# Optimization experiments

Measured on AMD Instinct MI355X. Metric: run time of the kernel, lower is better.

Reference implementation:

```python
import jax, jax.numpy as jnp
import numpy as np

B, N, C = 2, 2048, 512
H = 8
HD = C // H


def _xavier(key, shape):
    fan_in, fan_out = shape[-1], shape[-2] if len(shape) > 1 else shape[-1]
    limit = float(np.sqrt(6.0 / (fan_in + fan_out)))
    return jax.random.uniform(key, shape, jnp.float32, -limit, limit)


def setup_inputs() -> dict:
    key = jax.random.key(0)
    ks = jax.random.split(key, 8)
    return {
        "x": jax.random.normal(ks[0], (B, N, C), jnp.float32),
        "pos_embedding": jax.random.normal(ks[1], (B, N, C), jnp.float32),
        "Wqkv": _xavier(ks[2], (3 * C, C)),      # nn.Linear(dim, 3*dim, bias=False)
        "Wpos": _xavier(ks[3], (C, C)),          # pos_proj, bias=False
        "u_bias": _xavier(ks[4], (H, HD)),
        "v_bias": _xavier(ks[5], (H, HD)),
        "Wproj": _xavier(ks[6], (C, C)),
        "bproj": jnp.zeros((C,), jnp.float32),
    }


def _relative_shift(ps):
    # ps: [B, H, N, M]
    b, h, n, m = ps.shape
    ps = jnp.pad(ps, ((0, 0), (0, 0), (0, 0), (1, 0)))  # zero column in front
    ps = ps.reshape(b, h, m + 1, n)[:, :, 1:, :]
    return ps.reshape(b, h, n, m)


def reference(x, pos_embedding, Wqkv, Wpos, u_bias, v_bias, Wproj, bproj):
    b, n, c = x.shape
    scale = HD ** -0.5
    qkv = (x @ Wqkv.T).reshape(b, n, 3, H, HD)
    q = qkv[:, :, 0].transpose(0, 2, 1, 3)  # [B,H,N,HD]
    k = qkv[:, :, 1].transpose(0, 2, 1, 3)
    v = qkv[:, :, 2].transpose(0, 2, 1, 3)
    pos = (pos_embedding @ Wpos.T).reshape(b, -1, H, HD)  # [B,M,H,HD]

    # content score: (q + u_bias) @ k^T -> [B,H,N,N]
    content = jnp.einsum("bhnd,bhmd->bhnm", q + u_bias[None, :, None, :], k)
    # pos score: (q + v_bias) @ pos^T -> [B,H,N,M]
    pos_score = jnp.einsum("bhnd,bmhd->bhnm", q + v_bias[None, :, None, :], pos)
    pos_score = _relative_shift(pos_score)

    attn = jax.nn.softmax((pos_score + content) * scale, axis=-1)
    out = jnp.einsum("bhnm,bhmd->bhnd", attn, v)
    out = out.transpose(0, 2, 1, 3).reshape(b, n, c)
    return out @ Wproj.T + bproj
```

## Files before the change

### kernel.cpp

```cpp
#include <hip/hip_runtime.h>

typedef __attribute__((ext_vector_type(8))) short bf16x8;
typedef __attribute__((ext_vector_type(4))) short bf16x4;
typedef __attribute__((ext_vector_type(4))) float f32x4;

__device__ __forceinline__ float bf2f(unsigned short u) {
  union { unsigned int i; float f; } c; c.i = ((unsigned int)u) << 16; return c.f;
}
__device__ __forceinline__ unsigned short f2bf(float x) {
  union { float f; unsigned int i; } c; c.f = x;
  return (unsigned short)((c.i + 0x7fffu + ((c.i >> 16) & 1u)) >> 16);
}
__device__ __forceinline__ unsigned int pk2(float a, float b) {
  return (unsigned int)f2bf(a) | ((unsigned int)f2bf(b) << 16);
}

__device__ __forceinline__ uint4 ld8f(const float* p) {
  const float4 a = *(const float4*)p;
  const float4 b = *(const float4*)(p + 4);
  uint4 r;
  r.x = (unsigned)f2bf(a.x) | ((unsigned)f2bf(a.y) << 16);
  r.y = (unsigned)f2bf(a.z) | ((unsigned)f2bf(a.w) << 16);
  r.z = (unsigned)f2bf(b.x) | ((unsigned)f2bf(b.y) << 16);
  r.w = (unsigned)f2bf(b.z) | ((unsigned)f2bf(b.w) << 16);
  return r;
}

__device__ __forceinline__ void gload16(const unsigned short* g, short* l) {
  __builtin_amdgcn_global_load_lds((const __attribute__((address_space(1))) void*)g,
                                   (__attribute__((address_space(3))) void*)l, 16, 0, 0);
}

__global__ __launch_bounds__(256) void k_cvt(const float* __restrict__ x,
    const float* __restrict__ pe, const float* __restrict__ wq,
    const float* __restrict__ wp, const float* __restrict__ wj,
    unsigned short* __restrict__ dst) {
  const long long i8 = ((long long)blockIdx.x * 256 + threadIdx.x) * 8;
  const float* src; long long off;
  if (i8 < 2097152)      { src = x;  off = i8; }
  else if (i8 < 4194304) { src = pe; off = i8 - 2097152; }
  else if (i8 < 4980736) { src = wq; off = i8 - 4194304; }
  else if (i8 < 5242880) { src = wp; off = i8 - 4980736; }
  else                   { src = wj; off = i8 - 5242880; }
  *(uint4*)&dst[i8] = ld8f(src + off);
}

__device__ __forceinline__ void gemm128_mainloop(const unsigned short* __restrict__ Arow,
                                                 const unsigned short* __restrict__ Wrow,
                                                 short* Asl, short* Wsl, f32x4 acc[4][4]) {
  const int tid = threadIdx.x, w = tid >> 6, lane = tid & 63, lm = lane & 15, lq = lane >> 4;
  const int wm = w >> 1, wn = w & 1;
  const int lrow = lane >> 3;
  const int gcol = (((lane & 7) ^ lrow) * 8);
#pragma unroll
  for (int mt = 0; mt < 4; ++mt)
#pragma unroll
    for (int nt = 0; nt < 4; ++nt) acc[mt][nt] = (f32x4){0.f, 0.f, 0.f, 0.f};
#pragma unroll 1
  for (int kc = 0; kc < 512; kc += 64) {
    __syncthreads();
#pragma unroll
    for (int ld = 0; ld < 4; ++ld) {
      const int rbase = w * 32 + ld * 8;
      gload16(&Arow[(size_t)(rbase + lrow) * 512 + kc + gcol], &Asl[rbase * 64]);
      gload16(&Wrow[(size_t)(rbase + lrow) * 512 + kc + gcol], &Wsl[rbase * 64]);
    }
    __syncthreads();
#pragma unroll
    for (int kk = 0; kk < 2; ++kk) {
      const int pcs = ((kk * 4 + lq) ^ (lm & 7)) * 8;
      bf16x8 af[4], bfr[4];
#pragma unroll
      for (int mt = 0; mt < 4; ++mt)
        af[mt] = *(const bf16x8*)&Asl[(wm * 64 + mt * 16 + lm) * 64 + pcs];
#pragma unroll
      for (int nt = 0; nt < 4; ++nt)
        bfr[nt] = *(const bf16x8*)&Wsl[(wn * 64 + nt * 16 + lm) * 64 + pcs];
#pragma unroll
      for (int mt = 0; mt < 4; ++mt)
#pragma unroll
        for (int nt = 0; nt < 4; ++nt)
          acc[mt][nt] = __builtin_amdgcn_mfma_f32_16x16x32_bf16(af[mt], bfr[nt], acc[mt][nt], 0, 0, 0);
    }
  }
}

__global__ __launch_bounds__(256) void k_gemm_qkvpos(const unsigned short* __restrict__ xb,
    const unsigned short* __restrict__ peb, const unsigned short* __restrict__ wqb,
    const unsigned short* __restrict__ wpb, const float* __restrict__ ub,
    const float* __restrict__ vb, unsigned short* __restrict__ qu,
    unsigned short* __restrict__ qv, unsigned short* __restrict__ kg,
    unsigned short* __restrict__ vg, unsigned short* __restrict__ pos) {
  __shared__ short Asl[128 * 64], Wsl[128 * 64];
  f32x4 acc[4][4];
  const int m0 = blockIdx.y * 128, cc0 = blockIdx.x * 128;
  const unsigned short* Arow = (cc0 < 1536 ? xb : peb) + (size_t)m0 * 512;
  const unsigned short* Wrow = (cc0 < 1536) ? (wqb + (size_t)cc0 * 512)
                                            : (wpb + (size_t)(cc0 - 1536) * 512);
  gemm128_mainloop(Arow, Wrow, Asl, Wsl, acc);
  const int tid = threadIdx.x, w = tid >> 6, lane = tid & 63, lm = lane & 15, lq = lane >> 4;
  const int wm = w >> 1, wn = w & 1;
#pragma unroll
  for (int nt = 0; nt < 4; ++nt) {
    const int cc = cc0 + wn * 64 + nt * 16 + lm;
    const int sec = cc >> 9, rem = cc & 511, h = rem >> 6, d = rem & 63;
#pragma unroll
    for (int mt = 0; mt < 4; ++mt) {
#pragma unroll
      for (int r = 0; r < 4; ++r) {
        const int m = m0 + wm * 64 + mt * 16 + lq * 4 + r;
        const int b = m >> 11, n = m & 2047;
        const size_t idx = ((size_t)(b * 8 + h) * 2048 + n) * 64 + d;
        const float val = acc[mt][nt][r];
        if (sec == 0) {
          qu[idx] = f2bf(val + ub[rem]);
          qv[idx] = f2bf(val + vb[rem]);
        } else if (sec == 1) {
          kg[idx] = f2bf(val);
        } else if (sec == 2) {
          vg[idx] = f2bf(val);
        } else {
          pos[idx] = f2bf(val);
        }
      }
    }
  }
}

__global__ __launch_bounds__(256) void k_transpose_v(const unsigned short* __restrict__ vg,
                                                     unsigned short* __restrict__ vt) {
  __shared__ short T[64][72];
  const int tid = threadIdx.x, bhid = blockIdx.y, n0 = blockIdx.x * 64;
#pragma unroll
  for (int s = 0; s < 2; ++s) {
    int u = tid + s * 256, row = u >> 3, c8 = (u & 7) * 8;
    *(uint4*)&T[row][c8] = *(const uint4*)&vg[((size_t)bhid * 2048 + n0 + row) * 64 + c8];
  }
  __syncthreads();
#pragma unroll
  for (int s = 0; s < 2; ++s) {
    int u = tid + s * 256, d = u >> 3, n8 = (u & 7) * 8;
    alignas(16) unsigned short tmp[8];
#pragma unroll
    for (int jj = 0; jj < 8; ++jj) tmp[jj] = (unsigned short)T[n8 + jj][d];
    *(uint4*)&vt[((size_t)bhid * 64 + d) * 2048 + n0 + n8] = *(const uint4*)tmp;
  }
}

__global__ __launch_bounds__(256, 2) void k_flash(const unsigned short* __restrict__ qu,
    const unsigned short* __restrict__ qv, const unsigned short* __restrict__ kg,
    const unsigned short* __restrict__ vt, const unsigned short* __restrict__ posg,
    unsigned short* __restrict__ og) {
  __shared__ short SB[23892];
  short* Ks = SB;
  short* Vs = SB + 4608;
  short* Pn = SB + 9216;
  short* T  = SB + 18432;
  float* Ored = (float*)SB;
  const int tid = threadIdx.x, w = tid >> 6, lane = tid & 63, lm = lane & 15, lq = lane >> 4;
  const int bh = blockIdx.y, i0 = blockIdx.x * 64;
  const size_t bhs = (size_t)bh;
  const unsigned short* qub = qu + bhs * (2048 * 64);
  const unsigned short* qvb = qv + bhs * (2048 * 64);
  const unsigned short* pob = posg + bhs * (2048 * 64);
  bf16x8 au[4][2];
#pragma unroll
  for (int qt = 0; qt < 4; ++qt) {
    au[qt][0] = *(const bf16x8*)&qub[(size_t)(i0 + qt * 16 + lm) * 64 + lq * 8];
    au[qt][1] = *(const bf16x8*)&qub[(size_t)(i0 + qt * 16 + lm) * 64 + 32 + lq * 8];
  }
  const bf16x8 av0 = *(const bf16x8*)&qvb[(size_t)(i0 + w * 16 + lm) * 64 + lq * 8];
  const bf16x8 av1 = *(const bf16x8*)&qvb[(size_t)(i0 + w * 16 + lm) * 64 + 32 + lq * 8];
  const int rowe = min(i0 + 49 + lm, 2047);
  const bf16x8 ae0 = *(const bf16x8*)&qvb[(size_t)rowe * 64 + lq * 8];
  const bf16x8 ae1 = *(const bf16x8*)&qvb[(size_t)rowe * 64 + 32 + lq * 8];
  float lsum[4] = {0.f, 0.f, 0.f, 0.f};
  f32x4 oacc[4][4];
#pragma unroll
  for (int ii = 0; ii < 4; ++ii)
#pragma unroll
    for (int jj = 0; jj < 4; ++jj) oacc[ii][jj] = (f32x4){0.f, 0.f, 0.f, 0.f};
  const int krow = tid >> 3, kc8 = (tid & 7) * 8;
  const int pb0 = 1983 - i0;
  uint4 kr0 = *(const uint4*)&kg[(bhs * 2048 + krow) * 64 + kc8];
  uint4 kr1 = *(const uint4*)&kg[(bhs * 2048 + krow + 32) * 64 + kc8];
  uint4 vr0 = *(const uint4*)&vt[(bhs * 64 + krow) * 2048 + kc8];
  uint4 vr1 = *(const uint4*)&vt[(bhs * 64 + krow + 32) * 2048 + kc8];
  uint4 pr[4];
#pragma unroll
  for (int s = 0; s < 4; ++s) {
    int u = tid + s * 256, prow = u >> 3, c8 = (u & 7) * 8;
    int grow = (pb0 + prow + 4096) & 2047;
    pr[s] = *(const uint4*)&pob[(size_t)grow * 64 + c8];
  }
#pragma unroll 1
  for (int jt = 0; jt < 32; ++jt) {
    const int j0 = jt * 64;
    const int pb = pb0 + j0;
    __syncthreads();
    *(uint4*)&Ks[krow * 72 + kc8] = kr0;
    *(uint4*)&Ks[(krow + 32) * 72 + kc8] = kr1;
    *(uint4*)&Vs[krow * 72 + kc8] = vr0;
    *(uint4*)&Vs[(krow + 32) * 72 + kc8] = vr1;
    if (jt == 0) {
#pragma unroll
      for (int s = 0; s < 4; ++s) {
        int u = tid + s * 256, prow = u >> 3, c8 = (u & 7) * 8;
        int slot = (pb + prow) & 127;
        *(uint4*)&Pn[slot * 72 + c8] = pr[s];
      }
    } else {
#pragma unroll
      for (int s = 0; s < 2; ++s) {
        int u = tid + s * 256, prow = u >> 3, c8 = (u & 7) * 8;
        int slot = (pb + 64 + prow) & 127;
        *(uint4*)&Pn[slot * 72 + c8] = pr[s];
      }
    }
    __syncthreads();
    if (jt < 31) {
      const int jn = j0 + 64;
      kr0 = *(const uint4*)&kg[(bhs * 2048 + jn + krow) * 64 + kc8];
      kr1 = *(const uint4*)&kg[(bhs * 2048 + jn + krow + 32) * 64 + kc8];
      vr0 = *(const uint4*)&vt[(bhs * 64 + krow) * 2048 + jn + kc8];
      vr1 = *(const uint4*)&vt[(bhs * 64 + krow + 32) * 2048 + jn + kc8];
#pragma unroll
      for (int s = 0; s < 2; ++s) {
        int u = tid + s * 256, prow = u >> 3, c8 = (u & 7) * 8;
        int grow = (pb + 128 + prow + 4096) & 2047;
        pr[s] = *(const uint4*)&pob[(size_t)grow * 64 + c8];
      }
    }
    const bf16x8 k0 = *(const bf16x8*)&Ks[(w * 16 + lm) * 72 + lq * 8];
    const bf16x8 k1 = *(const bf16x8*)&Ks[(w * 16 + lm) * 72 + 32 + lq * 8];
    f32x4 cacc[4];
#pragma unroll
    for (int qt = 0; qt < 4; ++qt) {
      cacc[qt] = __builtin_amdgcn_mfma_f32_16x16x32_bf16(k0, au[qt][0], (f32x4){0.f,0.f,0.f,0.f}, 0, 0, 0);
      cacc[qt] = __builtin_amdgcn_mfma_f32_16x16x32_bf16(k1, au[qt][1], cacc[qt], 0, 0, 0);
    }
    const int sbase = 49 - w * 16;
#pragma unroll
    for (int ct = 0; ct < 5; ++ct) {
      const int slot = (pb + sbase + ct * 16 + lm) & 127;
      const bf16x8 b0 = *(const bf16x8*)&Pn[slot * 72 + lq * 8];
      const bf16x8 b1 = *(const bf16x8*)&Pn[slot * 72 + 32 + lq * 8];
      f32x4 t0 = __builtin_amdgcn_mfma_f32_16x16x32_bf16(b0, av0, (f32x4){0.f,0.f,0.f,0.f}, 0, 0, 0);
      t0 = __builtin_amdgcn_mfma_f32_16x16x32_bf16(b1, av1, t0, 0, 0, 0);
      uint2 pk; pk.x = pk2(t0[0], t0[1]); pk.y = pk2(t0[2], t0[3]);
      *(uint2*)&T[(w * 16 + lm) * 84 + ct * 16 + lq * 4] = pk;
    }
    {
      const int slot = (pb + w * 16 + lm) & 127;
      const bf16x8 b0 = *(const bf16x8*)&Pn[slot * 72 + lq * 8];
      const bf16x8 b1 = *(const bf16x8*)&Pn[slot * 72 + 32 + lq * 8];
      f32x4 e0 = __builtin_amdgcn_mfma_f32_16x16x32_bf16(b0, ae0, (f32x4){0.f,0.f,0.f,0.f}, 0, 0, 0);
      e0 = __builtin_amdgcn_mfma_f32_16x16x32_bf16(b1, ae1, e0, 0, 0, 0);
      if (lm == 15) {
        uint2 pk; pk.x = pk2(e0[0], e0[1]); pk.y = pk2(e0[2], e0[3]);
        *(uint2*)&T[64 * 84 + w * 16 + lq * 4] = pk;
      }
    }
    __syncthreads();
    const int diag = i0 - j0;
    const int jl0 = w * 16 + lq * 4;
    bf16x4 pf[4];
    if (diag >= 64 || diag <= -128) {
      const int du = (diag <= -128) ? 1 : 0;
      const int rm = lm + du;
#pragma unroll
      for (int qt = 0; qt < 4; ++qt) {
        const int rowa = qt * 16 + rm;
        const int base = (rowa == 64) ? (64 * 84 + jl0)
                                      : (rowa * 84 + 15 + jl0 - (rm & 15));
#pragma unroll
        for (int r = 0; r < 4; ++r) {
          const float pv = bf2f((unsigned short)T[base + r]);
          const float p = exp2f((cacc[qt][r] + pv) * 0.18033688f);
          lsum[qt] += p;
          pf[qt][r] = (short)f2bf(p);
        }
      }
    } else {
#pragma unroll
      for (int qt = 0; qt < 4; ++qt) {
#pragma unroll
        for (int r = 0; r < 4; ++r) {
          const int jl = jl0 + r;
          const int d = (j0 - i0) + jl - (qt * 16 + lm);
          float pv;
          if (d == 1) {
            pv = 0.f;
          } else {
            const int rm2 = lm + ((d > 1) ? 1 : 0);
            const int rowa = qt * 16 + rm2;
            const int base = (rowa == 64) ? (64 * 84 + jl)
                                          : (rowa * 84 + 15 + jl - (rm2 & 15));
            pv = bf2f((unsigned short)T[base]);
          }
          const float p = exp2f((cacc[qt][r] + pv) * 0.18033688f);
          lsum[qt] += p;
          pf[qt][r] = (short)f2bf(p);
        }
      }
    }
#pragma unroll
    for (int dt = 0; dt < 4; ++dt) {
      const bf16x4 vf = *(const bf16x4*)&Vs[(dt * 16 + lm) * 72 + w * 16 + lq * 4];
#pragma unroll
      for (int qt = 0; qt < 4; ++qt)
        oacc[qt][dt] = __builtin_amdgcn_mfma_f32_16x16x16bf16_1k(pf[qt], vf, oacc[qt][dt], 0, 0, 0);
    }
  }
#pragma unroll
  for (int qt = 0; qt < 4; ++qt) {
    lsum[qt] += __shfl_xor(lsum[qt], 16, 64);
    lsum[qt] += __shfl_xor(lsum[qt], 32, 64);
  }
  __syncthreads();
  if (w == 0) {
#pragma unroll
    for (int qt = 0; qt < 4; ++qt) {
#pragma unroll
      for (int dt = 0; dt < 4; ++dt)
        *(f32x4*)&Ored[(dt * 16 + lm) * 68 + qt * 16 + lq * 4] = oacc[qt][dt];
      if (lq == 0) Ored[64 * 68 + qt * 16 + lm] = lsum[qt];
    }
  }
  __syncthreads();
#pragma unroll 1
  for (int ww = 1; ww < 4; ++ww) {
    if (w == ww) {
#pragma unroll
      for (int qt = 0; qt < 4; ++qt) {
#pragma unroll
        for (int dt = 0; dt < 4; ++dt) {
          f32x4 o = *(const f32x4*)&Ored[(dt * 16 + lm) * 68 + qt * 16 + lq * 4];
          o += oacc[qt][dt];
          *(f32x4*)&Ored[(dt * 16 + lm) * 68 + qt * 16 + lq * 4] = o;
        }
        if (lq == 0) Ored[64 * 68 + qt * 16 + lm] += lsum[qt];
      }
    }
    __syncthreads();
  }
  const int b = bh >> 3, h = bh & 7;
  const f32x4 lv = *(const f32x4*)&Ored[64 * 68 + w * 16 + lq * 4];
  f32x4 inv;
#pragma unroll
  for (int r = 0; r < 4; ++r) inv[r] = 1.f / lv[r];
#pragma unroll
  for (int dt = 0; dt < 4; ++dt) {
    const f32x4 o = *(const f32x4*)&Ored[(dt * 16 + lm) * 68 + w * 16 + lq * 4];
#pragma unroll
    for (int r = 0; r < 4; ++r)
      og[((size_t)b * 2048 + i0 + w * 16 + lq * 4 + r) * 512 + h * 64 + dt * 16 + lm] =
          f2bf(o[r] * inv[r]);
  }
}

__global__ __launch_bounds__(256) void k_gemm_proj(const unsigned short* __restrict__ og,
    const unsigned short* __restrict__ wjb, const float* __restrict__ bproj,
    float* __restrict__ out) {
  __shared__ short Asl[128 * 64], Wsl[128 * 64];
  f32x4 acc[4][4];
  const int m0 = blockIdx.y * 128, cc0 = blockIdx.x * 128;
  gemm128_mainloop(og + (size_t)m0 * 512, wjb + (size_t)cc0 * 512, Asl, Wsl, acc);
  const int tid = threadIdx.x, w = tid >> 6, lane = tid & 63, lm = lane & 15, lq = lane >> 4;
  const int wm = w >> 1, wn = w & 1;
#pragma unroll
  for (int nt = 0; nt < 4; ++nt) {
    const int cc = cc0 + wn * 64 + nt * 16 + lm;
    const float bias = bproj[cc];
#pragma unroll
    for (int mt = 0; mt < 4; ++mt) {
#pragma unroll
      for (int r = 0; r < 4; ++r) {
        const int m = m0 + wm * 64 + mt * 16 + lq * 4 + r;
        out[(size_t)m * 512 + cc] = acc[mt][nt][r] + bias;
      }
    }
  }
}

extern "C" void kernel_launch(void* const* d_in, const int* in_sizes, int n_in,
                              void* d_out, int out_size, void* d_ws, size_t ws_size,
                              hipStream_t stream) {
  const float* x     = (const float*)d_in[0];
  const float* pe    = (const float*)d_in[1];
  const float* wqkv  = (const float*)d_in[2];
  const float* wpos  = (const float*)d_in[3];
  const float* ub    = (const float*)d_in[4];
  const float* vb    = (const float*)d_in[5];
  const float* wproj = (const float*)d_in[6];
  const float* bproj = (const float*)d_in[7];
  float* out = (float*)d_out;
  unsigned short* ws = (unsigned short*)d_ws;

  const size_t SZ = (size_t)2 * 8 * 2048 * 64;
  unsigned short* qu   = ws;
  unsigned short* qv   = qu + SZ;
  unsigned short* kg   = qv + SZ;
  unsigned short* vg   = kg + SZ;
  unsigned short* vt   = vg + SZ;
  unsigned short* pos  = vt + SZ;
  unsigned short* og   = pos + SZ;
  unsigned short* cvtb = og + SZ;
  unsigned short* xb   = cvtb;
  unsigned short* peb  = cvtb + 2097152;
  unsigned short* wqb  = cvtb + 4194304;
  unsigned short* wpb  = cvtb + 4980736;
  unsigned short* wjb  = cvtb + 5242880;

  dim3 blk(256);
  hipLaunchKernelGGL(k_cvt,         dim3(2688),   blk, 0, stream, x, pe, wqkv, wpos, wproj, cvtb);
  hipLaunchKernelGGL(k_gemm_qkvpos, dim3(16, 32), blk, 0, stream,
                     xb, peb, wqb, wpb, ub, vb, qu, qv, kg, vg, pos);
  hipLaunchKernelGGL(k_transpose_v, dim3(32, 16), blk, 0, stream, vg, vt);
  hipLaunchKernelGGL(k_flash,       dim3(32, 16), blk, 0, stream, qu, qv, kg, vt, pos, og);
  hipLaunchKernelGGL(k_gemm_proj,   dim3(4, 32),  blk, 0, stream, og, wjb, bproj, out);
}
```

Measured before the change: 227.0 us.

## Halve flash query tile, drop pos LDS ring, remap blocks for locality

Shrinks the flash attention query tile from 64 to 32 rows, doubling the grid to 1024 blocks and raising the occupancy hint to 4 blocks per CU with a smaller shared buffer. The staged positional-embedding ring buffer in LDS is removed; waves read pos rows straight from global memory and split the relative-position MFMA work between wave pairs. Block indices are remapped so neighbouring blocks share a head pair, aiming at better cache reuse. The costs are that K/V tiles are loaded twice as often per query row and pos reads go through global/L2 instead of LDS.

```diff
diff --git a/kernel.cpp b/kernel.cpp
--- a/kernel.cpp
+++ b/kernel.cpp
@@ -147,37 +147,40 @@
   }
 }
 
-__global__ __launch_bounds__(256, 2) void k_flash(const unsigned short* __restrict__ qu,
+__global__ __launch_bounds__(256, 4) void k_flash(const unsigned short* __restrict__ qu,
     const unsigned short* __restrict__ qv, const unsigned short* __restrict__ kg,
     const unsigned short* __restrict__ vt, const unsigned short* __restrict__ posg,
     unsigned short* __restrict__ og) {
-  __shared__ short SB[23892];
+  __shared__ short SB[11988];
   short* Ks = SB;
   short* Vs = SB + 4608;
-  short* Pn = SB + 9216;
-  short* T  = SB + 18432;
+  short* T  = SB + 9216;
   float* Ored = (float*)SB;
   const int tid = threadIdx.x, w = tid >> 6, lane = tid & 63, lm = lane & 15, lq = lane >> 4;
-  const int bh = blockIdx.y, i0 = blockIdx.x * 64;
+  const int hw = blockIdx.x + 64 * blockIdx.y;
+  const int idx = hw >> 3;
+  const int bh = (hw & 7) * 2 + (idx & 1);
+  const int i0 = (idx >> 1) * 32;
   const size_t bhs = (size_t)bh;
   const unsigned short* qub = qu + bhs * (2048 * 64);
   const unsigned short* qvb = qv + bhs * (2048 * 64);
   const unsigned short* pob = posg + bhs * (2048 * 64);
-  bf16x8 au[4][2];
-#pragma unroll
-  for (int qt = 0; qt < 4; ++qt) {
+  bf16x8 au[2][2];
+#pragma unroll
+  for (int qt = 0; qt < 2; ++qt) {
     au[qt][0] = *(const bf16x8*)&qub[(size_t)(i0 + qt * 16 + lm) * 64 + lq * 8];
     au[qt][1] = *(const bf16x8*)&qub[(size_t)(i0 + qt * 16 + lm) * 64 + 32 + lq * 8];
   }
-  const bf16x8 av0 = *(const bf16x8*)&qvb[(size_t)(i0 + w * 16 + lm) * 64 + lq * 8];
-  const bf16x8 av1 = *(const bf16x8*)&qvb[(size_t)(i0 + w * 16 + lm) * 64 + 32 + lq * 8];
-  const int rowe = min(i0 + 49 + lm, 2047);
+  const int sw = w >> 1, ph = w & 1;
+  const bf16x8 av0 = *(const bf16x8*)&qvb[(size_t)(i0 + sw * 16 + lm) * 64 + lq * 8];
+  const bf16x8 av1 = *(const bf16x8*)&qvb[(size_t)(i0 + sw * 16 + lm) * 64 + 32 + lq * 8];
+  const int rowe = min(i0 + 17 + lm, 2047);
   const bf16x8 ae0 = *(const bf16x8*)&qvb[(size_t)rowe * 64 + lq * 8];
   const bf16x8 ae1 = *(const bf16x8*)&qvb[(size_t)rowe * 64 + 32 + lq * 8];
-  float lsum[4] = {0.f, 0.f, 0.f, 0.f};
-  f32x4 oacc[4][4];
-#pragma unroll
-  for (int ii = 0; ii < 4; ++ii)
+  float lsum[2] = {0.f, 0.f};
+  f32x4 oacc[2][4];
+#pragma unroll
+  for (int ii = 0; ii < 2; ++ii)
 #pragma unroll
     for (int jj = 0; jj < 4; ++jj) oacc[ii][jj] = (f32x4){0.f, 0.f, 0.f, 0.f};
   const int krow = tid >> 3, kc8 = (tid & 7) * 8;
@@ -186,13 +189,6 @@
   uint4 kr1 = *(const uint4*)&kg[(bhs * 2048 + krow + 32) * 64 + kc8];
   uint4 vr0 = *(const uint4*)&vt[(bhs * 64 + krow) * 2048 + kc8];
   uint4 vr1 = *(const uint4*)&vt[(bhs * 64 + krow + 32) * 2048 + kc8];
-  uint4 pr[4];
-#pragma unroll
-  for (int s = 0; s < 4; ++s) {
-    int u = tid + s * 256, prow = u >> 3, c8 = (u & 7) * 8;
-    int grow = (pb0 + prow + 4096) & 2047;
-    pr[s] = *(const uint4*)&pob[(size_t)grow * 64 + c8];
-  }
 #pragma unroll 1
   for (int jt = 0; jt < 32; ++jt) {
     const int j0 = jt * 64;
@@ -202,21 +198,6 @@
     *(uint4*)&Ks[(krow + 32) * 72 + kc8] = kr1;
     *(uint4*)&Vs[krow * 72 + kc8] = vr0;
     *(uint4*)&Vs[(krow + 32) * 72 + kc8] = vr1;
-    if (jt == 0) {
-#pragma unroll
-      for (int s = 0; s < 4; ++s) {
-        int u = tid + s * 256, prow = u >> 3, c8 = (u & 7) * 8;
-        int slot = (pb + prow) & 127;
-        *(uint4*)&Pn[slot * 72 + c8] = pr[s];
-      }
-    } else {
-#pragma unroll
-      for (int s = 0; s < 2; ++s) {
-        int u = tid + s * 256, prow = u >> 3, c8 = (u & 7) * 8;
-        int slot = (pb + 64 + prow) & 127;
-        *(uint4*)&Pn[slot * 72 + c8] = pr[s];
-      }
-    }
     __syncthreads();
     if (jt < 31) {
       const int jn = j0 + 64;
@@ -224,54 +205,63 @@
       kr1 = *(const uint4*)&kg[(bhs * 2048 + jn + krow + 32) * 64 + kc8];
       vr0 = *(const uint4*)&vt[(bhs * 64 + krow) * 2048 + jn + kc8];
       vr1 = *(const uint4*)&vt[(bhs * 64 + krow + 32) * 2048 + jn + kc8];
-#pragma unroll
-      for (int s = 0; s < 2; ++s) {
-        int u = tid + s * 256, prow = u >> 3, c8 = (u & 7) * 8;
-        int grow = (pb + 128 + prow + 4096) & 2047;
-        pr[s] = *(const uint4*)&pob[(size_t)grow * 64 + c8];
-      }
     }
     const bf16x8 k0 = *(const bf16x8*)&Ks[(w * 16 + lm) * 72 + lq * 8];
     const bf16x8 k1 = *(const bf16x8*)&Ks[(w * 16 + lm) * 72 + 32 + lq * 8];
-    f32x4 cacc[4];
-#pragma unroll
-    for (int qt = 0; qt < 4; ++qt) {
+    f32x4 cacc[2];
+#pragma unroll
+    for (int qt = 0; qt < 2; ++qt) {
       cacc[qt] = __builtin_amdgcn_mfma_f32_16x16x32_bf16(k0, au[qt][0], (f32x4){0.f,0.f,0.f,0.f}, 0, 0, 0);
       cacc[qt] = __builtin_amdgcn_mfma_f32_16x16x32_bf16(k1, au[qt][1], cacc[qt], 0, 0, 0);
     }
-    const int sbase = 49 - w * 16;
-#pragma unroll
-    for (int ct = 0; ct < 5; ++ct) {
-      const int slot = (pb + sbase + ct * 16 + lm) & 127;
-      const bf16x8 b0 = *(const bf16x8*)&Pn[slot * 72 + lq * 8];
-      const bf16x8 b1 = *(const bf16x8*)&Pn[slot * 72 + 32 + lq * 8];
-      f32x4 t0 = __builtin_amdgcn_mfma_f32_16x16x32_bf16(b0, av0, (f32x4){0.f,0.f,0.f,0.f}, 0, 0, 0);
-      t0 = __builtin_amdgcn_mfma_f32_16x16x32_bf16(b1, av1, t0, 0, 0, 0);
-      uint2 pk; pk.x = pk2(t0[0], t0[1]); pk.y = pk2(t0[2], t0[3]);
-      *(uint2*)&T[(w * 16 + lm) * 84 + ct * 16 + lq * 4] = pk;
-    }
-    {
-      const int slot = (pb + w * 16 + lm) & 127;
-      const bf16x8 b0 = *(const bf16x8*)&Pn[slot * 72 + lq * 8];
-      const bf16x8 b1 = *(const bf16x8*)&Pn[slot * 72 + 32 + lq * 8];
-      f32x4 e0 = __builtin_amdgcn_mfma_f32_16x16x32_bf16(b0, ae0, (f32x4){0.f,0.f,0.f,0.f}, 0, 0, 0);
-      e0 = __builtin_amdgcn_mfma_f32_16x16x32_bf16(b1, ae1, e0, 0, 0, 0);
-      if (lm == 15) {
-        uint2 pk; pk.x = pk2(e0[0], e0[1]); pk.y = pk2(e0[2], e0[3]);
-        *(uint2*)&T[64 * 84 + w * 16 + lq * 4] = pk;
+    const int sbase = 49 - sw * 16;
+    if (ph == 0) {
+#pragma unroll
+      for (int ct = 0; ct < 3; ++ct) {
+        const int grow = (pb + sbase + ct * 16 + lm + 4096) & 2047;
+        const bf16x8 b0 = *(const bf16x8*)&pob[(size_t)grow * 64 + lq * 8];
+        const bf16x8 b1 = *(const bf16x8*)&pob[(size_t)grow * 64 + 32 + lq * 8];
+        f32x4 t0 = __builtin_amdgcn_mfma_f32_16x16x32_bf16(b0, av0, (f32x4){0.f,0.f,0.f,0.f}, 0, 0, 0);
+        t0 = __builtin_amdgcn_mfma_f32_16x16x32_bf16(b1, av1, t0, 0, 0, 0);
+        uint2 pk; pk.x = pk2(t0[0], t0[1]); pk.y = pk2(t0[2], t0[3]);
+        *(uint2*)&T[(sw * 16 + lm) * 84 + ct * 16 + lq * 4] = pk;
+      }
+    } else {
+#pragma unroll
+      for (int ct = 3; ct < 5; ++ct) {
+        const int grow = (pb + sbase + ct * 16 + lm + 4096) & 2047;
+        const bf16x8 b0 = *(const bf16x8*)&pob[(size_t)grow * 64 + lq * 8];
+        const bf16x8 b1 = *(const bf16x8*)&pob[(size_t)grow * 64 + 32 + lq * 8];
+        f32x4 t0 = __builtin_amdgcn_mfma_f32_16x16x32_bf16(b0, av0, (f32x4){0.f,0.f,0.f,0.f}, 0, 0, 0);
+        t0 = __builtin_amdgcn_mfma_f32_16x16x32_bf16(b1, av1, t0, 0, 0, 0);
+        uint2 pk; pk.x = pk2(t0[0], t0[1]); pk.y = pk2(t0[2], t0[3]);
+        *(uint2*)&T[(sw * 16 + lm) * 84 + ct * 16 + lq * 4] = pk;
+      }
+#pragma unroll
+      for (int e = 0; e < 2; ++e) {
+        const int ee = sw * 2 + e;
+        const int grow = (pb + 32 + ee * 16 + lm + 4096) & 2047;
+        const bf16x8 b0 = *(const bf16x8*)&pob[(size_t)grow * 64 + lq * 8];
+        const bf16x8 b1 = *(const bf16x8*)&pob[(size_t)grow * 64 + 32 + lq * 8];
+        f32x4 e0 = __builtin_amdgcn_mfma_f32_16x16x32_bf16(b0, ae0, (f32x4){0.f,0.f,0.f,0.f}, 0, 0, 0);
+        e0 = __builtin_amdgcn_mfma_f32_16x16x32_bf16(b1, ae1, e0, 0, 0, 0);
+        if (lm == 15) {
+          uint2 pk; pk.x = pk2(e0[0], e0[1]); pk.y = pk2(e0[2], e0[3]);
+          *(uint2*)&T[32 * 84 + ee * 16 + lq * 4] = pk;
+        }
       }
     }
     __syncthreads();
     const int diag = i0 - j0;
     const int jl0 = w * 16 + lq * 4;
-    bf16x4 pf[4];
-    if (diag >= 64 || diag <= -128) {
-      const int du = (diag <= -128) ? 1 : 0;
+    bf16x4 pf[2];
+    if (diag >= 64 || diag <= -64) {
+      const int du = (diag <= -64) ? 1 : 0;
       const int rm = lm + du;
 #pragma unroll
-      for (int qt = 0; qt < 4; ++qt) {
+      for (int qt = 0; qt < 2; ++qt) {
         const int rowa = qt * 16 + rm;
-        const int base = (rowa == 64) ? (64 * 84 + jl0)
+        const int base = (rowa == 32) ? (32 * 84 + jl0)
                                       : (rowa * 84 + 15 + jl0 - (rm & 15));
 #pragma unroll
         for (int r = 0; r < 4; ++r) {
@@ -283,7 +273,7 @@
       }
     } else {
 #pragma unroll
-      for (int qt = 0; qt < 4; ++qt) {
+      for (int qt = 0; qt < 2; ++qt) {
 #pragma unroll
         for (int r = 0; r < 4; ++r) {
           const int jl = jl0 + r;
@@ -294,7 +284,7 @@
           } else {
             const int rm2 = lm + ((d > 1) ? 1 : 0);
             const int rowa = qt * 16 + rm2;
-            const int base = (rowa == 64) ? (64 * 84 + jl)
+            const int base = (rowa == 32) ? (32 * 84 + jl)
                                           : (rowa * 84 + 15 + jl - (rm2 & 15));
             pv = bf2f((unsigned short)T[base]);
           }
@@ -307,24 +297,23 @@
 #pragma unroll
     for (int dt = 0; dt < 4; ++dt) {
       const bf16x4 vf = *(const bf16x4*)&Vs[(dt * 16 + lm) * 72 + w * 16 + lq * 4];
-#pragma unroll
-      for (int qt = 0; qt < 4; ++qt)
-        oacc[qt][dt] = __builtin_amdgcn_mfma_f32_16x16x16bf16_1k(pf[qt], vf, oacc[qt][dt], 0, 0, 0);
-    }
-  }
-#pragma unroll
-  for (int qt = 0; qt < 4; ++qt) {
+      oacc[0][dt] = __builtin_amdgcn_mfma_f32_16x16x16bf16_1k(pf[0], vf, oacc[0][dt], 0, 0, 0);
+      oacc[1][dt] = __builtin_amdgcn_mfma_f32_16x16x16bf16_1k(pf[1], vf, oacc[1][dt], 0, 0, 0);
+    }
+  }
+#pragma unroll
+  for (int qt = 0; qt < 2; ++qt) {
     lsum[qt] += __shfl_xor(lsum[qt], 16, 64);
     lsum[qt] += __shfl_xor(lsum[qt], 32, 64);
   }
   __syncthreads();
   if (w == 0) {
 #pragma unroll
-    for (int qt = 0; qt < 4; ++qt) {
+    for (int qt = 0; qt < 2; ++qt) {
 #pragma unroll
       for (int dt = 0; dt < 4; ++dt)
-        *(f32x4*)&Ored[(dt * 16 + lm) * 68 + qt * 16 + lq * 4] = oacc[qt][dt];
-      if (lq == 0) Ored[64 * 68 + qt * 16 + lm] = lsum[qt];
+        *(f32x4*)&Ored[(dt * 16 + lm) * 36 + qt * 16 + lq * 4] = oacc[qt][dt];
+      if (lq == 0) Ored[64 * 36 + qt * 16 + lm] = lsum[qt];
     }
   }
   __syncthreads();
@@ -332,30 +321,32 @@
   for (int ww = 1; ww < 4; ++ww) {
     if (w == ww) {
 #pragma unroll
-      for (int qt = 0; qt < 4; ++qt) {
+      for (int qt = 0; qt < 2; ++qt) {
 #pragma unroll
         for (int dt = 0; dt < 4; ++dt) {
-          f32x4 o = *(const f32x4*)&Ored[(dt * 16 + lm) * 68 + qt * 16 + lq * 4];
+          f32x4 o = *(const f32x4*)&Ored[(dt * 16 + lm) * 36 + qt * 16 + lq * 4];
           o += oacc[qt][dt];
-          *(f32x4*)&Ored[(dt * 16 + lm) * 68 + qt * 16 + lq * 4] = o;
+          *(f32x4*)&Ored[(dt * 16 + lm) * 36 + qt * 16 + lq * 4] = o;
         }
-        if (lq == 0) Ored[64 * 68 + qt * 16 + lm] += lsum[qt];
-      }
-    }
-    __syncthreads();
-  }
-  const int b = bh >> 3, h = bh & 7;
-  const f32x4 lv = *(const f32x4*)&Ored[64 * 68 + w * 16 + lq * 4];
-  f32x4 inv;
-#pragma unroll
-  for (int r = 0; r < 4; ++r) inv[r] = 1.f / lv[r];
-#pragma unroll
-  for (int dt = 0; dt < 4; ++dt) {
-    const f32x4 o = *(const f32x4*)&Ored[(dt * 16 + lm) * 68 + w * 16 + lq * 4];
-#pragma unroll
-    for (int r = 0; r < 4; ++r)
-      og[((size_t)b * 2048 + i0 + w * 16 + lq * 4 + r) * 512 + h * 64 + dt * 16 + lm] =
-          f2bf(o[r] * inv[r]);
+        if (lq == 0) Ored[64 * 36 + qt * 16 + lm] += lsum[qt];
+      }
+    }
+    __syncthreads();
+  }
+  if (w < 2) {
+    const int b = bh >> 3, h = bh & 7;
+    const f32x4 lv = *(const f32x4*)&Ored[64 * 36 + w * 16 + lq * 4];
+    f32x4 inv;
+#pragma unroll
+    for (int r = 0; r < 4; ++r) inv[r] = 1.f / lv[r];
+#pragma unroll
+    for (int dt = 0; dt < 4; ++dt) {
+      const f32x4 o = *(const f32x4*)&Ored[(dt * 16 + lm) * 36 + w * 16 + lq * 4];
+#pragma unroll
+      for (int r = 0; r < 4; ++r)
+        og[((size_t)b * 2048 + i0 + w * 16 + lq * 4 + r) * 512 + h * 64 + dt * 16 + lm] =
+            f2bf(o[r] * inv[r]);
+    }
   }
 }
 
@@ -417,6 +408,6 @@
   hipLaunchKernelGGL(k_gemm_qkvpos, dim3(16, 32), blk, 0, stream,
                      xb, peb, wqb, wpb, ub, vb, qu, qv, kg, vg, pos);
   hipLaunchKernelGGL(k_transpose_v, dim3(32, 16), blk, 0, stream, vg, vt);
-  hipLaunchKernelGGL(k_flash,       dim3(32, 16), blk, 0, stream, qu, qv, kg, vt, pos, og);
+  hipLaunchKernelGGL(k_flash,       dim3(64, 16), blk, 0, stream, qu, qv, kg, vt, pos, og);
   hipLaunchKernelGGL(k_gemm_proj,   dim3(4, 32),  blk, 0, stream, og, wjb, bproj, out);
 }
```

Result: slower. 253.2 us (+11.5%).
